# Performance work log

Measured on AMD Instinct MI355X. Metric: run time of the kernel, lower is better.

## Reference

```python
import jax, jax.numpy as jnp
import numpy as np

EPS = 1e-5


def _corner_data(x, cmin, stride, D, H, W):
    # continuous grid indices (x_idx, y_idx, z_idx); index 0 = first voxel center
    idx = (x - cmin[None, :]) / stride[None, :]
    gx, gy, gz = idx[:, 0], idx[:, 1], idx[:, 2]
    x0 = jnp.floor(gx); y0 = jnp.floor(gy); z0 = jnp.floor(gz)
    fx = jnp.clip(gx - x0, 0.0, 1.0)
    fy = jnp.clip(gy - y0, 0.0, 1.0)
    fz = jnp.clip(gz - z0, 0.0, 1.0)
    x0i = x0.astype(jnp.int32); x1i = x0i + 1
    y0i = y0.astype(jnp.int32); y1i = y0i + 1
    z0i = z0.astype(jnp.int32); z1i = z0i + 1
    # 8 trilinear corners, same order as the torch reference
    xs = jnp.stack([x0i, x1i, x0i, x1i, x0i, x1i, x0i, x1i])
    ys = jnp.stack([y0i, y0i, y1i, y1i, y0i, y0i, y1i, y1i])
    zs = jnp.stack([z0i, z0i, z0i, z0i, z1i, z1i, z1i, z1i])
    wx = jnp.stack([1 - fx, fx, 1 - fx, fx, 1 - fx, fx, 1 - fx, fx])
    wy = jnp.stack([1 - fy, 1 - fy, fy, fy, 1 - fy, 1 - fy, fy, fy])
    wz = jnp.stack([1 - fz, 1 - fz, 1 - fz, 1 - fz, fz, fz, fz, fz])
    ws = wx * wy * wz                                    # (8, N)
    valid = (xs >= 0) & (xs < W) & (ys >= 0) & (ys < H) & (zs >= 0) & (zs < D)
    xi = jnp.clip(xs, 0, W - 1)
    yi = jnp.clip(ys, 0, H - 1)
    zi = jnp.clip(zs, 0, D - 1)
    flat = zi * (H * W) + yi * W + xi                    # (8, N) flat voxel index
    return flat, ws * valid.astype(ws.dtype)


def setup_inputs() -> dict:
    key = jax.random.key(0)
    ks = jax.random.split(key, 20)
    N = 200000; B = 4; D = H = W = 64; CG = 64; NC = 128; HID = 128
    h = jax.random.normal(ks[0], (N, NC), jnp.float32)
    x = jax.random.uniform(ks[1], (N, 3), jnp.float32) * 63.0
    grid = jax.random.normal(ks[2], (B, CG, D, H, W), jnp.float32)
    node_batch = jax.random.randint(ks[3], (N,), 0, B, jnp.int32)
    coordinates_min = jnp.zeros((3,), jnp.float32)
    spatial_stride = jnp.ones((3,), jnp.float32)
    s = 0.05
    params = dict(
        w1=jax.random.normal(ks[4], (HID, NC + CG), jnp.float32) * s,
        b1=jax.random.normal(ks[5], (HID,), jnp.float32) * s,
        w2=jax.random.normal(ks[6], (NC, HID), jnp.float32) * s,
        b2=jax.random.normal(ks[7], (NC,), jnp.float32) * s,
        ln_g=1.0 + jax.random.normal(ks[8], (NC,), jnp.float32) * s,
        ln_b=jax.random.normal(ks[9], (NC,), jnp.float32) * s,
        wn2g=jax.random.normal(ks[10], (CG, NC), jnp.float32) * s,
        bn2g=jax.random.normal(ks[11], (CG,), jnp.float32) * s,
        wc1=jax.random.normal(ks[12], (CG, 2 * CG), jnp.float32) * s,
        bc1=jax.random.normal(ks[13], (CG,), jnp.float32) * s,
        wc2=jax.random.normal(ks[14], (CG, CG), jnp.float32) * s,
        bc2=jax.random.normal(ks[15], (CG,), jnp.float32) * s,
        in_g=1.0 + jax.random.normal(ks[16], (CG,), jnp.float32) * s,
        in_b=jax.random.normal(ks[17], (CG,), jnp.float32) * s,
    )
    return dict(h=h, x=x, grid=grid, node_batch=node_batch,
                coordinates_min=coordinates_min, spatial_stride=spatial_stride, **params)


def reference(h, x, grid, node_batch, coordinates_min, spatial_stride,
              w1, b1, w2, b2, ln_g, ln_b, wn2g, bn2g, wc1, bc1, wc2, bc2, in_g, in_b):
    B, Cg, D, H, W = grid.shape
    DHW = D * H * W
    flat, w = _corner_data(x, coordinates_min, spatial_stride, D, H, W)  # (8,N)

    # grid -> node: trilinear gather (== grid_sample, align_corners=True, zeros padding)
    gflat = grid.reshape(B, Cg, DHW).transpose(0, 2, 1)                  # (B,DHW,Cg)
    vals = gflat[node_batch[None, :], flat]                              # (8,N,Cg)
    sampled = jnp.einsum('kn,knc->nc', w, vals)                          # (N,Cg)

    # node MLP + residual + LayerNorm
    z = jnp.concatenate([h, sampled], axis=-1)
    m = jax.nn.silu(z @ w1.T + b1) @ w2.T + b2
    hn = h + m
    mu = hn.mean(-1, keepdims=True)
    var = hn.var(-1, keepdims=True)
    hn = (hn - mu) / jnp.sqrt(var + EPS) * ln_g + ln_b

    # node -> grid: trilinear scatter-add splat of projected features
    proj = hn @ wn2g.T + bn2g                                            # (N,Cg)
    gidx = node_batch[None, :] * DHW + flat                              # (8,N) global flat index
    contrib = w[:, :, None] * proj[None]                                 # (8,N,Cg)
    vol = jnp.zeros((B * DHW, Cg), grid.dtype).at[gidx.reshape(-1)].add(contrib.reshape(-1, Cg))
    splat = vol.reshape(B, D, H, W, Cg).transpose(0, 4, 1, 2, 3)         # (B,Cg,D,H,W)

    # grid MLP (1x1x1 convs) + residual + InstanceNorm (affine)
    cat = jnp.concatenate([grid, splat], axis=1)                         # (B,2Cg,D,H,W)
    g1 = jax.nn.silu(jnp.einsum('bcdhw,oc->bodhw', cat, wc1) + bc1[None, :, None, None, None])
    g2 = jnp.einsum('bcdhw,oc->bodhw', g1, wc2) + bc2[None, :, None, None, None]
    gr = grid + g2
    mu = gr.mean((2, 3, 4), keepdims=True)
    var = gr.var((2, 3, 4), keepdims=True)
    gr = (gr - mu) / jnp.sqrt(var + EPS) * in_g[None, :, None, None, None] + in_b[None, :, None, None, None]
    return hn, gr
```

## Files before the change

kernel.cpp:

```cpp
#include <hip/hip_runtime.h>
#include <hip/hip_fp16.h>
#include <cstdint>

#define NNODES 200000
#define NCH 128
#define NBATCH 4
#define DHW 262144
#define K1 192

#define VOLH_OFF  0ull
#define VOLH_BYTES 134217728ull
#define PART_OFF  134217728ull
#define STAT_OFF  142606336ull
#define NWF_OFF   142608384ull
#define WF_OFF    142706688ull
#define GT_OFF    257931264ull
#define GRH_OFF   392149056ull

typedef _Float16 h2 __attribute__((ext_vector_type(2)));
typedef __fp16  fp16x2 __attribute__((ext_vector_type(2)));
typedef _Float16 f16x8 __attribute__((ext_vector_type(8)));
typedef float f32x4 __attribute__((ext_vector_type(4)));

__device__ __forceinline__ uint32_t pack_h2(float a, float b){
  fp16x2 p = __builtin_amdgcn_cvt_pkrtz(a, b);
  return __builtin_bit_cast(uint32_t, p);
}
__device__ __forceinline__ h2 as_h2(uint32_t w){ return __builtin_bit_cast(h2, w); }
__device__ __forceinline__ float siluf(float a){ return a / (1.f + __expf(-a)); }
__device__ __forceinline__ f32x4 mfma16(uint4 a, uint4 b, f32x4 c){
  return __builtin_amdgcn_mfma_f32_16x16x32_f16(
      __builtin_bit_cast(f16x8, a), __builtin_bit_cast(f16x8, b), c, 0, 0, 0);
}
__device__ __forceinline__ void atomic_pk_add_f16(uint32_t* addr, uint32_t val){
  asm volatile("global_atomic_pk_add_f16 %0, %1, off"
               :: "v"(addr), "v"(val) : "memory");
}

__global__ void pack_all(const float* __restrict__ w1, const float* __restrict__ w2,
                         const float* __restrict__ wn2g,
                         const float* __restrict__ wc1, const float* __restrict__ wc2,
                         uint32_t* __restrict__ nwf, uint32_t* __restrict__ wf)
{
  int t = blockIdx.x * 256 + threadIdx.x;
  if (t < 24576) {
    int q = t & 3, lane = (t >> 2) & 63;
    int vl = lane & 15, g = lane >> 4;
    if (t < 12288) {
      int f = t >> 8, s = f % 6, tt = f / 6;
      int o = tt * 16 + vl, k = s * 32 + g * 8 + 2 * q;
      nwf[t] = pack_h2(w1[o * K1 + k], w1[o * K1 + k + 1]);
    } else if (t < 20480) {
      int f = (t - 12288) >> 8, s = f & 3, tt = f >> 2;
      int o = tt * 16 + vl, k = s * 32 + g * 8 + 2 * q;
      nwf[t] = pack_h2(w2[o * 128 + k], w2[o * 128 + k + 1]);
    } else {
      int f = (t - 20480) >> 8, s = f & 3, tt = f >> 2;
      int o = tt * 16 + vl, k = s * 32 + g * 8 + 2 * q;
      nwf[t] = pack_h2(wn2g[o * 128 + k], wn2g[o * 128 + k + 1]);
    }
  } else if (t < 30720) {
    int u = t - 24576;
    if (u < 4096) {
      int q = u & 3, lane = (u >> 2) & 63, f = u >> 8;
      int s = f & 3, tt = f >> 2;
      int o = tt * 16 + (lane & 15);
      int k = s * 32 + (lane >> 4) * 8 + 2 * q;
      wf[u] = pack_h2(wc1[o * 128 + k], wc1[o * 128 + k + 1]);
    } else {
      int uu = u - 4096;
      int q = uu & 3, lane = (uu >> 2) & 63, f = uu >> 8;
      int s = f & 1, tt = f >> 1;
      int o = tt * 16 + (lane & 15);
      int k = s * 32 + (lane >> 4) * 8 + 2 * q;
      wf[u] = pack_h2(wc2[o * 64 + k], wc2[o * 64 + k + 1]);
    }
  }
}

__global__ void transpose_kernel(const float* __restrict__ grid, uint32_t* __restrict__ gt,
                                 uint4* __restrict__ volz)
{
  __shared__ float tile[64][65];
  {
    size_t base = (size_t)blockIdx.x * 512 + threadIdx.x;
    const uint4 z = make_uint4(0u, 0u, 0u, 0u);
    volz[base] = z;
    volz[base + 256] = z;
  }
  int bx = blockIdx.x;
  int b = bx >> 12;
  int dhw0 = (bx & 4095) << 6;
  const float* gbase = grid + ((size_t)b * 64) * DHW + dhw0;
  int c0 = threadIdx.x >> 6, d = threadIdx.x & 63;
  #pragma unroll
  for (int i = 0; i < 16; ++i)
    tile[i * 4 + c0][d] = gbase[(size_t)(i * 4 + c0) * DHW + d];
  __syncthreads();
  uint32_t* tb = gt + ((size_t)b * DHW + dhw0) * 32;
  int p = threadIdx.x & 31, r0 = threadIdx.x >> 5;
  #pragma unroll
  for (int i = 0; i < 8; ++i) {
    int dd = i * 8 + r0;
    tb[(size_t)dd * 32 + p] = pack_h2(tile[2 * p][dd], tile[2 * p + 1][dd]);
  }
}

__launch_bounds__(512, 1)
__global__ void node_fused(const float* __restrict__ h, const float* __restrict__ x,
                           const uint32_t* __restrict__ gridT, const int* __restrict__ nbat,
                           const float* __restrict__ cmin, const float* __restrict__ sstr,
                           const uint32_t* __restrict__ nwf,
                           const float* __restrict__ b1, const float* __restrict__ b2,
                           const float* __restrict__ ln_g, const float* __restrict__ ln_b,
                           const float* __restrict__ bn2g,
                           float* __restrict__ hn_out, uint32_t* __restrict__ volh)
{
  __shared__ __align__(16) uint32_t zt[64][100];
  __shared__ __align__(16) uint32_t g1z[64][68];
  __shared__ float wpart[8][64][2];
  __shared__ float cwS[64][8];
  __shared__ int   cfS[64][8];

  const int tid = threadIdx.x;
  const int lane = tid & 63, w = tid >> 6;
  const int g = lane >> 4, vl = lane & 15;
  const int n0 = blockIdx.x * 64;

  const uint4* nf4 = (const uint4*)nwf;
  uint4 a1f[6], a2f[4], apf[4];
  #pragma unroll
  for (int s = 0; s < 6; ++s) a1f[s] = nf4[(w * 6 + s) * 64 + lane];
  #pragma unroll
  for (int s = 0; s < 4; ++s) a2f[s] = nf4[3072 + (w * 4 + s) * 64 + lane];
  #pragma unroll
  for (int s = 0; s < 4; ++s) apf[s] = nf4[5120 + ((w & 3) * 4 + s) * 64 + lane];

  const int cbase = w * 16 + g * 4;
  float4 b1r = *(const float4*)&b1[cbase];
  float4 b2r = *(const float4*)&b2[cbase];
  float4 lgr = *(const float4*)&ln_g[cbase];
  float4 lbr = *(const float4*)&ln_b[cbase];
  float4 bnr = *(const float4*)&bn2g[(w & 3) * 16 + g * 4];

  {
    const float c0 = cmin[0], c1 = cmin[1], c2 = cmin[2];
    const float st0 = sstr[0], st1 = sstr[1], st2 = sstr[2];
    int nd = tid & 63, k = tid >> 6;
    int n = n0 + nd;
    float gx = (x[n * 3 + 0] - c0) / st0;
    float gy = (x[n * 3 + 1] - c1) / st1;
    float gz = (x[n * 3 + 2] - c2) / st2;
    float fx0 = floorf(gx), fy0 = floorf(gy), fz0 = floorf(gz);
    float fx = fminf(fmaxf(gx - fx0, 0.f), 1.f);
    float fy = fminf(fmaxf(gy - fy0, 0.f), 1.f);
    float fz = fminf(fmaxf(gz - fz0, 0.f), 1.f);
    int ix0 = (int)fx0, iy0 = (int)fy0, iz0 = (int)fz0;
    int b = nbat[n];
    int xi = (k & 1) ? ix0 + 1 : ix0;
    int yi = (k & 2) ? iy0 + 1 : iy0;
    int zi = (k & 4) ? iz0 + 1 : iz0;
    float wx = (k & 1) ? fx : 1.f - fx;
    float wy = (k & 2) ? fy : 1.f - fy;
    float wz = (k & 4) ? fz : 1.f - fz;
    bool valid = (xi >= 0) & (xi < 64) & (yi >= 0) & (yi < 64) & (zi >= 0) & (zi < 64);
    int xc = min(max(xi, 0), 63), yc = min(max(yi, 0), 63), zc = min(max(zi, 0), 63);
    cwS[nd][k] = valid ? wx * wy * wz : 0.f;
    cfS[nd][k] = b * DHW + ((zc << 12) | (yc << 6) | xc);
  }
  {
    int nd = tid >> 3, o = tid & 7;
    const float4* hp = (const float4*)&h[(size_t)(n0 + nd) * NCH + o * 16];
    #pragma unroll
    for (int u = 0; u < 4; ++u) {
      float4 f = hp[u];
      zt[nd][o * 8 + 2 * u]     = pack_h2(f.x, f.y);
      zt[nd][o * 8 + 2 * u + 1] = pack_h2(f.z, f.w);
    }
  }
  __syncthreads();

  {
    const int p = lane & 31, kb = lane >> 5;
    #pragma unroll 4
    for (int i = 0; i < 8; ++i) {
      int nd = w * 8 + i;
      float slo = 0.f, shi = 0.f;
      #pragma unroll
      for (int jj = 0; jj < 4; ++jj) {
        int k = 2 * jj + kb;
        int   cfk = cfS[nd][k];
        float cwk = cwS[nd][k];
        h2 gv = as_h2(gridT[(size_t)cfk * 32 + p]);
        slo = fmaf(cwk, (float)gv.x, slo);
        shi = fmaf(cwk, (float)gv.y, shi);
      }
      slo += __shfl_xor(slo, 32);
      shi += __shfl_xor(shi, 32);
      if (lane < 32) zt[nd][64 + p] = pack_h2(slo, shi);
    }
  }
  __syncthreads();

  #pragma unroll
  for (int nc = 0; nc < 4; ++nc) {
    uint4 bfr[6];
    #pragma unroll
    for (int s = 0; s < 6; ++s) bfr[s] = *(const uint4*)&zt[nc * 16 + vl][s * 16 + g * 4];
    f32x4 acc;
    acc[0] = b1r.x; acc[1] = b1r.y; acc[2] = b1r.z; acc[3] = b1r.w;
    #pragma unroll
    for (int s = 0; s < 6; ++s) acc = mfma16(a1f[s], bfr[s], acc);
    uint2 pr;
    pr.x = pack_h2(siluf(acc[0]), siluf(acc[1]));
    pr.y = pack_h2(siluf(acc[2]), siluf(acc[3]));
    *(uint2*)&g1z[nc * 16 + vl][w * 8 + g * 2] = pr;
  }
  __syncthreads();

  float hnv[4][4];
  #pragma unroll
  for (int nc = 0; nc < 4; ++nc) {
    uint4 bfr[4];
    #pragma unroll
    for (int s = 0; s < 4; ++s) bfr[s] = *(const uint4*)&g1z[nc * 16 + vl][s * 16 + g * 4];
    f32x4 acc;
    acc[0] = b2r.x; acc[1] = b2r.y; acc[2] = b2r.z; acc[3] = b2r.w;
    #pragma unroll
    for (int s = 0; s < 4; ++s) acc = mfma16(a2f[s], bfr[s], acc);
    uint2 hp = *(const uint2*)&zt[nc * 16 + vl][w * 8 + g * 2];
    h2 p0 = as_h2(hp.x), p1 = as_h2(hp.y);
    float v0 = acc[0] + (float)p0.x;
    float v1 = acc[1] + (float)p0.y;
    float v2 = acc[2] + (float)p1.x;
    float v3 = acc[3] + (float)p1.y;
    hnv[nc][0] = v0; hnv[nc][1] = v1; hnv[nc][2] = v2; hnv[nc][3] = v3;
    float s_ = v0 + v1 + v2 + v3;
    float q_ = v0 * v0 + v1 * v1 + v2 * v2 + v3 * v3;
    s_ += __shfl_xor(s_, 16); q_ += __shfl_xor(q_, 16);
    s_ += __shfl_xor(s_, 32); q_ += __shfl_xor(q_, 32);
    if (lane < 16) { wpart[w][nc * 16 + lane][0] = s_; wpart[w][nc * 16 + lane][1] = q_; }
  }
  __syncthreads();

  #pragma unroll
  for (int nc = 0; nc < 4; ++nc) {
    int node = nc * 16 + vl;
    float ssum = 0.f, qsum = 0.f;
    #pragma unroll
    for (int ww = 0; ww < 8; ++ww) {
      float2 pp = *(const float2*)&wpart[ww][node][0];
      ssum += pp.x; qsum += pp.y;
    }
    float mu = ssum * (1.f / 128.f);
    float var = qsum * (1.f / 128.f) - mu * mu;
    float rstd = rsqrtf(var + 1e-5f);
    float y0 = (hnv[nc][0] - mu) * rstd * lgr.x + lbr.x;
    float y1 = (hnv[nc][1] - mu) * rstd * lgr.y + lbr.y;
    float y2 = (hnv[nc][2] - mu) * rstd * lgr.z + lbr.z;
    float y3 = (hnv[nc][3] - mu) * rstd * lgr.w + lbr.w;
    *(float4*)&hn_out[(size_t)(n0 + node) * NCH + cbase] = make_float4(y0, y1, y2, y3);
    uint2 pz;
    pz.x = pack_h2(y0, y1);
    pz.y = pack_h2(y2, y3);
    *(uint2*)&g1z[node][w * 8 + g * 2] = pz;
  }
  __syncthreads();

  #pragma unroll
  for (int ncq = 0; ncq < 2; ++ncq) {
    int nc = (w >> 2) * 2 + ncq;
    int node = nc * 16 + vl;
    uint4 bfr[4];
    #pragma unroll
    for (int s = 0; s < 4; ++s) bfr[s] = *(const uint4*)&g1z[node][s * 16 + g * 4];
    f32x4 acc;
    acc[0] = bnr.x; acc[1] = bnr.y; acc[2] = bnr.z; acc[3] = bnr.w;
    #pragma unroll
    for (int s = 0; s < 4; ++s) acc = mfma16(apf[s], bfr[s], acc);
    uint2 pr;
    pr.x = pack_h2(acc[0], acc[1]);
    pr.y = pack_h2(acc[2], acc[3]);
    *(uint2*)&zt[node][(w & 3) * 8 + g * 2] = pr;
  }
  __syncthreads();

  {
    const int half = lane >> 5, c = lane & 31;
    for (int i = 0; i < 8; ++i) {
      int node = w * 8 + i;
      uint32_t pz = zt[node][c];
      h2 p = as_h2(pz);
      #pragma unroll
      for (int kk = 0; kk < 4; ++kk) {
        int k = 2 * kk + half;
        float wv = cwS[node][k];
        if (wv != 0.f) {
          int gidx = cfS[node][k];
          uint32_t v = pack_h2(wv * (float)p.x, wv * (float)p.y);
          atomic_pk_add_f16(&volh[(size_t)gidx * 32 + c], v);
        }
      }
    }
  }
}

__launch_bounds__(256, 2)
__global__ void voxel_kernel(const uint32_t* __restrict__ gridT, const uint32_t* __restrict__ volh,
                             const uint32_t* __restrict__ wf, const float* __restrict__ bc1,
                             const float* __restrict__ bc2,
                             _Float16* __restrict__ grh, float* __restrict__ partials)
{
  __shared__ __align__(16) uint32_t xt[64][68];
  __shared__ __align__(16) uint32_t g1b[4][16][36];
  __shared__ float part_s[4][128];

  const int tid = threadIdx.x;
  const int lane = tid & 63, wv = tid >> 6;
  const int g = lane >> 4, vl = lane & 15;
  const int b = blockIdx.x >> 12;
  const int dhw0 = (blockIdx.x & 4095) << 6;

  {
    const uint32_t* gt = gridT + ((size_t)b * DHW + dhw0) * 32;
    #pragma unroll
    for (int it = 0; it < 2; ++it) {
      int u = it * 256 + tid;
      int v = u >> 3, p4 = u & 7;
      *(uint4*)&xt[v][4 * p4] = *(const uint4*)&gt[(size_t)v * 32 + 4 * p4];
    }
  }
  {
    const uint32_t* vb = volh + ((size_t)b * DHW + dhw0) * 32;
    #pragma unroll
    for (int it = 0; it < 2; ++it) {
      int u = it * 256 + tid;
      int v = u >> 3, p4 = u & 7;
      *(uint4*)&xt[v][32 + 4 * p4] = *(const uint4*)&vb[(size_t)v * 32 + 4 * p4];
    }
  }

  const uint4* wf4 = (const uint4*)wf;
  uint4 w1f[4][4], w2f[4][2];
  #pragma unroll
  for (int t = 0; t < 4; ++t)
    #pragma unroll
    for (int s = 0; s < 4; ++s)
      w1f[t][s] = wf4[(t * 4 + s) * 64 + lane];
  #pragma unroll
  for (int t = 0; t < 4; ++t)
    #pragma unroll
    for (int s = 0; s < 2; ++s)
      w2f[t][s] = wf4[1024 + (t * 2 + s) * 64 + lane];

  f32x4 acc1[4];
  #pragma unroll
  for (int t = 0; t < 4; ++t) {
    #pragma unroll
    for (int r = 0; r < 4; ++r) acc1[t][r] = bc1[t * 16 + g * 4 + r];
  }

  __syncthreads();

  const int v = wv * 16 + vl;
  #pragma unroll
  for (int s = 0; s < 4; ++s) {
    uint4 xb = *(const uint4*)&xt[v][s * 16 + g * 4];
    #pragma unroll
    for (int t = 0; t < 4; ++t) acc1[t] = mfma16(w1f[t][s], xb, acc1[t]);
  }

  #pragma unroll
  for (int t = 0; t < 4; ++t) {
    uint2 pr;
    pr.x = pack_h2(siluf(acc1[t][0]), siluf(acc1[t][1]));
    pr.y = pack_h2(siluf(acc1[t][2]), siluf(acc1[t][3]));
    *(uint2*)&g1b[wv][vl][t * 8 + g * 2] = pr;
  }
  asm volatile("s_waitcnt lgkmcnt(0)" ::: "memory");

  f32x4 acc2[4];
  #pragma unroll
  for (int t = 0; t < 4; ++t) {
    #pragma unroll
    for (int r = 0; r < 4; ++r) acc2[t][r] = bc2[t * 16 + g * 4 + r];
  }
  #pragma unroll
  for (int s = 0; s < 2; ++s) {
    uint4 gv = *(const uint4*)&g1b[wv][vl][s * 16 + g * 4];
    #pragma unroll
    for (int t = 0; t < 4; ++t) acc2[t] = mfma16(w2f[t][s], gv, acc2[t]);
  }

  const int dhw = dhw0 + v;
  #pragma unroll
  for (int t = 0; t < 4; ++t) {
    uint2 gp = *(const uint2*)&xt[v][t * 8 + g * 2];
    h2 g0 = as_h2(gp.x), g1 = as_h2(gp.y);
    float gc[4] = {(float)g0.x, (float)g0.y, (float)g1.x, (float)g1.y};
    #pragma unroll
    for (int r = 0; r < 4; ++r) {
      int o = t * 16 + g * 4 + r;
      float grv = gc[r] + acc2[t][r];
      grh[(size_t)(b * 64 + o) * DHW + dhw] = (_Float16)grv;
      float sv = grv, qv = grv * grv;
      sv += __shfl_xor(sv, 1, 64); qv += __shfl_xor(qv, 1, 64);
      sv += __shfl_xor(sv, 2, 64); qv += __shfl_xor(qv, 2, 64);
      sv += __shfl_xor(sv, 4, 64); qv += __shfl_xor(qv, 4, 64);
      sv += __shfl_xor(sv, 8, 64); qv += __shfl_xor(qv, 8, 64);
      if (vl == 0) { part_s[wv][2 * o] = sv; part_s[wv][2 * o + 1] = qv; }
    }
  }
  __syncthreads();
  if (tid < 128)
    partials[(size_t)blockIdx.x * 128 + tid] =
        part_s[0][tid] + part_s[1][tid] + part_s[2][tid] + part_s[3][tid];
}

__global__ void stats_kernel(const float* __restrict__ partials, const float* __restrict__ in_g,
                             const float* __restrict__ in_b, float* __restrict__ stats)
{
  int bo = blockIdx.x;
  int b = bo >> 6, o = bo & 63;
  float s = 0.f, q = 0.f;
  for (int k = threadIdx.x; k < 4096; k += 256) {
    const float* pp = partials + (size_t)(b * 4096 + k) * 128 + 2 * o;
    s += pp[0]; q += pp[1];
  }
  __shared__ float sred[256], qred[256];
  sred[threadIdx.x] = s; qred[threadIdx.x] = q;
  __syncthreads();
  for (int st = 128; st >= 1; st >>= 1) {
    if (threadIdx.x < st) { sred[threadIdx.x] += sred[threadIdx.x + st]; qred[threadIdx.x] += qred[threadIdx.x + st]; }
    __syncthreads();
  }
  if (threadIdx.x == 0) {
    float mu = sred[0] * (1.f / (float)DHW);
    float var = qred[0] * (1.f / (float)DHW) - mu * mu;
    float rstd = rsqrtf(var + 1e-5f);
    float scale = rstd * in_g[o];
    stats[2 * bo] = scale;
    stats[2 * bo + 1] = in_b[o] - mu * scale;
  }
}

__global__ void norm_kernel(const uint2* __restrict__ grh2, const float* __restrict__ stats,
                            float* __restrict__ gr)
{
  const size_t total = (size_t)NBATCH * 64 * DHW / 4;
  size_t stride = (size_t)gridDim.x * 256;
  for (size_t i = blockIdx.x * 256 + threadIdx.x; i < total; i += stride) {
    int bo = (int)(i >> 16);
    float scale = stats[2 * bo], shift = stats[2 * bo + 1];
    uint2 u = grh2[i];
    h2 p0 = as_h2(u.x), p1 = as_h2(u.y);
    float4 o;
    o.x = fmaf((float)p0.x, scale, shift);
    o.y = fmaf((float)p0.y, scale, shift);
    o.z = fmaf((float)p1.x, scale, shift);
    o.w = fmaf((float)p1.y, scale, shift);
    *(float4*)&gr[4 * i] = o;
  }
}

extern "C" void kernel_launch(void* const* d_in, const int* in_sizes, int n_in,
                              void* d_out, int out_size, void* d_ws, size_t ws_size,
                              hipStream_t stream)
{
  const float* h     = (const float*)d_in[0];
  const float* x     = (const float*)d_in[1];
  const float* grid  = (const float*)d_in[2];
  const int*   nbat  = (const int*)d_in[3];
  const float* cmin  = (const float*)d_in[4];
  const float* sstr  = (const float*)d_in[5];
  const float* w1    = (const float*)d_in[6];
  const float* b1    = (const float*)d_in[7];
  const float* w2    = (const float*)d_in[8];
  const float* b2    = (const float*)d_in[9];
  const float* ln_g  = (const float*)d_in[10];
  const float* ln_b  = (const float*)d_in[11];
  const float* wn2g  = (const float*)d_in[12];
  const float* bn2g  = (const float*)d_in[13];
  const float* wc1   = (const float*)d_in[14];
  const float* bc1   = (const float*)d_in[15];
  const float* wc2   = (const float*)d_in[16];
  const float* bc2   = (const float*)d_in[17];
  const float* in_g  = (const float*)d_in[18];
  const float* in_b  = (const float*)d_in[19];

  float* hn_out = (float*)d_out;
  float* gr_out = (float*)d_out + (size_t)NNODES * NCH;

  char* ws = (char*)d_ws;
  uint32_t* volh     = (uint32_t*)(ws + VOLH_OFF);
  float*    partials = (float*)(ws + PART_OFF);
  float*    stats    = (float*)(ws + STAT_OFF);
  uint32_t* nwf      = (uint32_t*)(ws + NWF_OFF);
  uint32_t* wf       = (uint32_t*)(ws + WF_OFF);
  uint32_t* gridT    = (uint32_t*)(ws + GT_OFF);
  _Float16* grh      = (_Float16*)(ws + GRH_OFF);

  pack_all<<<120, 256, 0, stream>>>(w1, w2, wn2g, wc1, wc2, nwf, wf);
  transpose_kernel<<<16384, 256, 0, stream>>>(grid, gridT, (uint4*)volh);
  node_fused<<<3125, 512, 0, stream>>>(h, x, gridT, nbat, cmin, sstr, nwf,
                                       b1, b2, ln_g, ln_b, bn2g, hn_out, volh);
  voxel_kernel<<<16384, 256, 0, stream>>>(gridT, volh, wf, bc1, bc2, grh, partials);
  stats_kernel<<<256, 256, 0, stream>>>(partials, in_g, in_b, stats);
  norm_kernel<<<8192, 256, 0, stream>>>((const uint2*)grh, stats, gr_out);
}
```

Before: 589.9 us.

## Replace global fp16 atomic splat with per-tile binned entries gathered in voxel kernel

Node kernel now writes projected features to a buffer and appends (node, voxel, weight) entries into fixed-capacity per-tile bins via a counter atomic, instead of issuing packed fp16 global atomics into a dense volume. The voxel kernel gathers its tile's entries, accumulates into shared-memory fp32 via LDS atomics, then packs into its input tile. This removes zeroing and reading a large dense volume and many global atomics, at the cost of random gathers of projected rows and a capacity limit that silently drops overflow entries.

```diff
diff --git a/kernel.cpp b/kernel.cpp
--- a/kernel.cpp
+++ b/kernel.cpp
@@ -7,15 +7,19 @@
 #define NBATCH 4
 #define DHW 262144
 #define K1 192
-
-#define VOLH_OFF  0ull
-#define VOLH_BYTES 134217728ull
-#define PART_OFF  134217728ull
-#define STAT_OFF  142606336ull
-#define NWF_OFF   142608384ull
-#define WF_OFF    142706688ull
-#define GT_OFF    257931264ull
-#define GRH_OFF   392149056ull
+#define NTILE 16384
+#define CAP 192
+
+#define ENT_OFF   0ull
+#define ENT_BYTES 25165824ull
+#define CNT_OFF   25165824ull
+#define PART_OFF  25231360ull
+#define STAT_OFF  33619968ull
+#define NWF_OFF   33622016ull
+#define WF_OFF    33720320ull
+#define PRJ_OFF   33744896ull
+#define GT_OFF    59344896ull
+#define GRH_OFF   193562624ull
 
 typedef _Float16 h2 __attribute__((ext_vector_type(2)));
 typedef __fp16  fp16x2 __attribute__((ext_vector_type(2)));
@@ -32,17 +36,15 @@
   return __builtin_amdgcn_mfma_f32_16x16x32_f16(
       __builtin_bit_cast(f16x8, a), __builtin_bit_cast(f16x8, b), c, 0, 0, 0);
 }
-__device__ __forceinline__ void atomic_pk_add_f16(uint32_t* addr, uint32_t val){
-  asm volatile("global_atomic_pk_add_f16 %0, %1, off"
-               :: "v"(addr), "v"(val) : "memory");
-}
 
 __global__ void pack_all(const float* __restrict__ w1, const float* __restrict__ w2,
                          const float* __restrict__ wn2g,
                          const float* __restrict__ wc1, const float* __restrict__ wc2,
-                         uint32_t* __restrict__ nwf, uint32_t* __restrict__ wf)
+                         uint32_t* __restrict__ nwf, uint32_t* __restrict__ wf,
+                         uint32_t* __restrict__ cnt)
 {
   int t = blockIdx.x * 256 + threadIdx.x;
+  if (t < NTILE) cnt[t] = 0u;
   if (t < 24576) {
     int q = t & 3, lane = (t >> 2) & 63;
     int vl = lane & 15, g = lane >> 4;
@@ -78,16 +80,9 @@
   }
 }
 
-__global__ void transpose_kernel(const float* __restrict__ grid, uint32_t* __restrict__ gt,
-                                 uint4* __restrict__ volz)
+__global__ void transpose_kernel(const float* __restrict__ grid, uint32_t* __restrict__ gt)
 {
   __shared__ float tile[64][65];
-  {
-    size_t base = (size_t)blockIdx.x * 512 + threadIdx.x;
-    const uint4 z = make_uint4(0u, 0u, 0u, 0u);
-    volz[base] = z;
-    volz[base + 256] = z;
-  }
   int bx = blockIdx.x;
   int b = bx >> 12;
   int dhw0 = (bx & 4095) << 6;
@@ -114,7 +109,8 @@
                            const float* __restrict__ b1, const float* __restrict__ b2,
                            const float* __restrict__ ln_g, const float* __restrict__ ln_b,
                            const float* __restrict__ bn2g,
-                           float* __restrict__ hn_out, uint32_t* __restrict__ volh)
+                           float* __restrict__ hn_out, uint32_t* __restrict__ prjv,
+                           uint2* __restrict__ entries, uint32_t* __restrict__ cnt)
 {
   __shared__ __align__(16) uint32_t zt[64][100];
   __shared__ __align__(16) uint32_t g1z[64][68];
@@ -281,32 +277,29 @@
     uint2 pr;
     pr.x = pack_h2(acc[0], acc[1]);
     pr.y = pack_h2(acc[2], acc[3]);
-    *(uint2*)&zt[node][(w & 3) * 8 + g * 2] = pr;
-  }
-  __syncthreads();
-
-  {
-    const int half = lane >> 5, c = lane & 31;
-    for (int i = 0; i < 8; ++i) {
-      int node = w * 8 + i;
-      uint32_t pz = zt[node][c];
-      h2 p = as_h2(pz);
-      #pragma unroll
-      for (int kk = 0; kk < 4; ++kk) {
-        int k = 2 * kk + half;
-        float wv = cwS[node][k];
-        if (wv != 0.f) {
-          int gidx = cfS[node][k];
-          uint32_t v = pack_h2(wv * (float)p.x, wv * (float)p.y);
-          atomic_pk_add_f16(&volh[(size_t)gidx * 32 + c], v);
-        }
-      }
+    *(uint2*)&prjv[(size_t)(n0 + node) * 32 + (w & 3) * 8 + g * 2] = pr;
+  }
+
+  {
+    int node_l = w * 8 + (lane >> 3);
+    int k = lane & 7;
+    float wv = cwS[node_l][k];
+    if (wv != 0.f) {
+      int gidx = cfS[node_l][k];
+      uint32_t t = (uint32_t)gidx >> 6;
+      uint32_t off = atomicAdd(&cnt[t], 1u);
+      if (off < CAP)
+        entries[(size_t)t * CAP + off] =
+            make_uint2(((uint32_t)(n0 + node_l) << 6) | ((uint32_t)gidx & 63u),
+                       __float_as_uint(wv));
     }
   }
 }
 
 __launch_bounds__(256, 2)
-__global__ void voxel_kernel(const uint32_t* __restrict__ gridT, const uint32_t* __restrict__ volh,
+__global__ void voxel_kernel(const uint32_t* __restrict__ gridT,
+                             const uint2* __restrict__ entries, const uint32_t* __restrict__ cnt,
+                             const uint32_t* __restrict__ prjv,
                              const uint32_t* __restrict__ wf, const float* __restrict__ bc1,
                              const float* __restrict__ bc2,
                              _Float16* __restrict__ grh, float* __restrict__ partials)
@@ -314,6 +307,7 @@
   __shared__ __align__(16) uint32_t xt[64][68];
   __shared__ __align__(16) uint32_t g1b[4][16][36];
   __shared__ float part_s[4][128];
+  __shared__ __align__(16) float vacc[64][64];
 
   const int tid = threadIdx.x;
   const int lane = tid & 63, wv = tid >> 6;
@@ -322,6 +316,12 @@
   const int dhw0 = (blockIdx.x & 4095) << 6;
 
   {
+    float4* vz = (float4*)&vacc[0][0];
+    const float4 z = make_float4(0.f, 0.f, 0.f, 0.f);
+    #pragma unroll
+    for (int i = 0; i < 4; ++i) vz[tid * 4 + i] = z;
+  }
+  {
     const uint32_t* gt = gridT + ((size_t)b * DHW + dhw0) * 32;
     #pragma unroll
     for (int it = 0; it < 2; ++it) {
@@ -330,15 +330,6 @@
       *(uint4*)&xt[v][4 * p4] = *(const uint4*)&gt[(size_t)v * 32 + 4 * p4];
     }
   }
-  {
-    const uint32_t* vb = volh + ((size_t)b * DHW + dhw0) * 32;
-    #pragma unroll
-    for (int it = 0; it < 2; ++it) {
-      int u = it * 256 + tid;
-      int v = u >> 3, p4 = u & 7;
-      *(uint4*)&xt[v][32 + 4 * p4] = *(const uint4*)&vb[(size_t)v * 32 + 4 * p4];
-    }
-  }
 
   const uint4* wf4 = (const uint4*)wf;
   uint4 w1f[4][4], w2f[4][2];
@@ -359,7 +350,31 @@
     #pragma unroll
     for (int r = 0; r < 4; ++r) acc1[t][r] = bc1[t * 16 + g * 4 + r];
   }
-
+  __syncthreads();
+
+  {
+    int n_e = min((int)cnt[blockIdx.x], CAP);
+    const uint2* ebase = entries + (size_t)blockIdx.x * CAP;
+    const int c = lane & 31;
+    for (int e = wv * 2 + (lane >> 5); e < n_e; e += 8) {
+      uint2 ent = ebase[e];
+      int xc = ent.x & 63;
+      int node = ent.x >> 6;
+      float wgt = __uint_as_float(ent.y);
+      uint32_t pv = prjv[(size_t)node * 32 + c];
+      h2 p = as_h2(pv);
+      atomicAdd(&vacc[xc][2 * c],     wgt * (float)p.x);
+      atomicAdd(&vacc[xc][2 * c + 1], wgt * (float)p.y);
+    }
+  }
+  __syncthreads();
+
+  {
+    int v = tid >> 2, pb = (tid & 3) * 8;
+    #pragma unroll
+    for (int i = 0; i < 8; ++i)
+      xt[v][32 + pb + i] = pack_h2(vacc[v][2 * (pb + i)], vacc[v][2 * (pb + i) + 1]);
+  }
   __syncthreads();
 
   const int v = wv * 16 + vl;
@@ -492,19 +507,23 @@
   float* gr_out = (float*)d_out + (size_t)NNODES * NCH;
 
   char* ws = (char*)d_ws;
-  uint32_t* volh     = (uint32_t*)(ws + VOLH_OFF);
+  uint2*    entries  = (uint2*)(ws + ENT_OFF);
+  uint32_t* cnt      = (uint32_t*)(ws + CNT_OFF);
   float*    partials = (float*)(ws + PART_OFF);
   float*    stats    = (float*)(ws + STAT_OFF);
   uint32_t* nwf      = (uint32_t*)(ws + NWF_OFF);
   uint32_t* wf       = (uint32_t*)(ws + WF_OFF);
+  uint32_t* prjv     = (uint32_t*)(ws + PRJ_OFF);
   uint32_t* gridT    = (uint32_t*)(ws + GT_OFF);
   _Float16* grh      = (_Float16*)(ws + GRH_OFF);
 
-  pack_all<<<120, 256, 0, stream>>>(w1, w2, wn2g, wc1, wc2, nwf, wf);
-  transpose_kernel<<<16384, 256, 0, stream>>>(grid, gridT, (uint4*)volh);
+  pack_all<<<120, 256, 0, stream>>>(w1, w2, wn2g, wc1, wc2, nwf, wf, cnt);
+  transpose_kernel<<<16384, 256, 0, stream>>>(grid, gridT);
   node_fused<<<3125, 512, 0, stream>>>(h, x, gridT, nbat, cmin, sstr, nwf,
-                                       b1, b2, ln_g, ln_b, bn2g, hn_out, volh);
-  voxel_kernel<<<16384, 256, 0, stream>>>(gridT, volh, wf, bc1, bc2, grh, partials);
+                                       b1, b2, ln_g, ln_b, bn2g, hn_out, prjv,
+                                       entries, cnt);
+  voxel_kernel<<<16384, 256, 0, stream>>>(gridT, entries, cnt, prjv, wf, bc1, bc2,
+                                          grh, partials);
   stats_kernel<<<256, 256, 0, stream>>>(partials, in_g, in_b, stats);
   norm_kernel<<<8192, 256, 0, stream>>>((const uint2*)grh, stats, gr_out);
 }
```

Result: slower. 1.024 ms (+73.6%).
